# Kernel optimization log

Measured on AMD Instinct MI355X. Metric: run time of the kernel, lower is better.

## Reference

```python
import jax, jax.numpy as jnp
import numpy as np
import math

ITERATIONS = 2
STRIDE = 1
ALPHA = 0.0
MEAN_DATA = 1.0
FINAL_LAMBDA = 0.01  # final_beta
EPS = 1e-7
MIN_VAR_ADD = 0.0005


def setup_inputs() -> dict:
    key = jax.random.key(0)
    k1, k2 = jax.random.split(key)
    b, h, w, k, i, o, a = 2, 12, 12, 3, 32, 32, 4
    votes = jax.random.normal(k1, (b, h, w, k, k, i, o, a, a), dtype=jnp.float32)
    acts = jax.random.uniform(k2, (b, h, w, k, k, i, 1, 1, 1), dtype=jnp.float32)
    beta_a = jnp.full((1, 1, 1, 1, 1, 1, o, 1, 1), 0.5, dtype=jnp.float32)
    beta_u = jnp.full((1, 1, 1, 1, 1, 1, o, 1, 1), 0.5, dtype=jnp.float32)
    return {"votes": votes, "acts": acts, "beta_a": beta_a, "beta_u": beta_u}


def reference(votes, acts, beta_a, beta_u):
    b, h, w, k = votes.shape[0], votes.shape[1], votes.shape[2], votes.shape[3]
    i, o, a = votes.shape[5], votes.shape[6], votes.shape[7]
    s = STRIDE
    Hr = h * s + k - s  # reconstructed height
    Wr = w * s + k - s
    # target spatial coords for each (h,y) / (w,x) of the kernel window
    Y = jnp.arange(h)[:, None] * s + jnp.arange(k)[None, :]  # (h,k)
    X = jnp.arange(w)[:, None] * s + jnp.arange(k)[None, :]  # (w,k)
    lin = (Y[:, None, :, None] * Wr + X[None, :, None, :]).reshape(-1)  # (h*w*k*k,)

    # R_ij init: softmax over zeros along out-capsule axis -> uniform 1/o
    R = jnp.full((b, h, w, k, k, i, o, 1, 1), 1.0 / o, dtype=votes.dtype)
    out_poses = jnp.zeros((b, h, w, 1, 1, 1, o, a, a), dtype=votes.dtype)

    def m_step(R, out_poses, it):
        Ra = R * acts                                   # (b,h,w,k,k,i,o,1,1)
        sumR = jnp.sum(Ra, axis=(3, 4, 5), keepdims=True)
        mu = jnp.sum(Ra * votes, axis=(3, 4, 5), keepdims=True) / (sumR + EPS)
        mu = (1.0 - ALPHA) * mu + ALPHA * out_poses     # (b,h,w,1,1,1,o,a,a)
        sig = jnp.sum(Ra * jnp.square(votes - mu), axis=(3, 4, 5), keepdims=True) / (sumR + EPS) + MIN_VAR_ADD
        cost = (beta_u - 0.5 * jnp.log(sig + EPS)) * sumR / MEAN_DATA
        inv_temp = FINAL_LAMBDA * (1.0 - 0.95 ** (it + 1))
        a_j = jax.nn.sigmoid(inv_temp * (beta_a - jnp.sum(cost, axis=(-1, -2), keepdims=True)))
        return mu, sig, a_j

    def e_step(mu, sig, a_j):
        log_p = -jnp.sum(jnp.log(2.0 * math.pi * sig) + jnp.square(votes - mu) / (2.0 * sig),
                         axis=(-1, -2), keepdims=True)        # (b,h,w,k,k,i,o,1,1)
        lognum = jnp.log(a_j) + log_p
        ap = jnp.exp(lognum - jnp.max(lognum))                # global-max shift as in original
        # scatter-add (fold / col2im) onto the reconstructed grid, then sum over o
        ap6 = ap.reshape(b, h, w, k, k, i, o)
        ap_t = ap6.transpose(1, 2, 3, 4, 0, 5, 6).reshape(h * w * k * k, b, i, o)
        dense = jax.ops.segment_sum(ap_t, lin, num_segments=Hr * Wr)  # (Hr*Wr,b,i,o)
        dense = dense.sum(-1).reshape(Hr, Wr, b, i)
        # extract_patches: gather the window sums back to (b,h,w,k,k,i)
        denom = dense[Y[:, None, :, None], X[None, :, None, :]]  # (h,w,k,k,b,i)
        denom = jnp.transpose(denom, (4, 0, 1, 2, 3, 5))[..., None, None, None]
        return ap / (denom + EPS)

    for it in range(ITERATIONS - 1):
        mu, sig, a_j = m_step(R, out_poses, it)
        out_poses = mu
        R = e_step(mu, sig, a_j)
    mu, sig, a_j = m_step(R, out_poses, ITERATIONS)

    poses = jnp.squeeze(mu, axis=(3, 4, 5))     # (b,h,w,o,a,a)
    acts_out = jnp.squeeze(a_j, axis=(3, 4, 5))  # (b,h,w,o,1,1)
    return poses, acts_out
```

## Files before the change

### kernel.cpp

```cpp
#include <hip/hip_runtime.h>
#include <math.h>

#define NB 2
#define NH 12
#define NW 12
#define NK 3
#define NI 32
#define NO 32
#define NA 16
#define NBHW (NB*NH*NW)
#define NC (NK*NK*NI)
#define CSTR (NO*NA)
#define VPB (NC*CSTR)
#define HR 14
#define WR 14
#define EPSF 1e-7f
#define MINVAR 5e-4f
#define TEMP0 0.0005f
#define TEMPF 0.00142625f

#define MU_OFF 0
#define W_OFF  147456
#define L_OFF  294912
#define BM_OFF 304128
#define M_OFF  304416
#define DENSE_OFF 304432
#define LOGNUM_OFF 316976
#define DENSE_N (NB*HR*WR*NI)

__global__ __launch_bounds__(256) void kA(const float* __restrict__ votes,
        const float* __restrict__ acts, const float* __restrict__ beta_a,
        const float* __restrict__ beta_u, float* __restrict__ ws) {
    __shared__ float s_acts[NC];
    const int bid = blockIdx.x;
    const int bhw = bid >> 1;
    const int obase = (bid & 1) * 16;
    const int t = threadIdx.x;
    const int a = t & 15;
    const int o = obase + (t >> 4);
    for (int idx = t; idx < NC; idx += 256) s_acts[idx] = acts[bhw*NC + idx];
    __syncthreads();
    const float* vb = votes + (size_t)bhw*VPB + obase*NA;
    float s1 = 0.f, s2 = 0.f, sumR = 0.f;
    #pragma unroll 4
    for (int c = 0; c < NC; ++c) {
        float v  = vb[(size_t)c*CSTR + t];
        float ra = s_acts[c] * (1.0f/NO);
        float rv = ra * v;
        s1 += rv;
        s2 = fmaf(rv, v, s2);
        sumR += ra;
    }
    float mu  = s1 / (sumR + EPSF);
    float sig = (s2 - mu*(2.f*s1 - mu*sumR)) / (sumR + EPSF) + MINVAR;
    ws[MU_OFF + bhw*512 + a*32 + o] = mu;
    ws[W_OFF  + bhw*512 + a*32 + o] = 0.5f / sig;
    float cost = (beta_u[o] - 0.5f*logf(sig + EPSF)) * sumR;
    float ps   = logf(6.2831853071795864f * sig);
    #pragma unroll
    for (int d = 1; d < 16; d <<= 1) {
        cost += __shfl_xor(cost, d);
        ps   += __shfl_xor(ps, d);
    }
    if (a == 0) {
        float aj = 1.0f/(1.0f + expf(-TEMP0*(beta_a[o] - cost)));
        ws[L_OFF + bhw*32 + o] = logf(aj) - ps;
    }
}

__global__ __launch_bounds__(256) void kB(const float* __restrict__ votes,
                                          float* __restrict__ ws) {
    const int bhw = blockIdx.x;
    const int t = threadIdx.x;
    const int o = t & 31;
    float mur[16], wr[16];
    const float* mup = ws + MU_OFF + bhw*512;
    const float* wp  = ws + W_OFF  + bhw*512;
    #pragma unroll
    for (int a = 0; a < 16; ++a) { mur[a] = mup[a*32+o]; wr[a] = wp[a*32+o]; }
    const float L = ws[L_OFF + bhw*32 + o];
    const float* vb = votes + (size_t)bhw*VPB;
    float* lp = ws + LOGNUM_OFF + (size_t)bhw*(NC*NO);
    float tmax = -3.0e38f;
    for (int it = 0; it < (NC*NO)/256/32*32/ (32/32); ) { break; }
    for (int it = 0; it < 36; ++it) {
        const int c = it*8 + (t >> 5);
        const float4* v4 = (const float4*)(vb + (size_t)c*CSTR + o*NA);
        float acc = 0.f;
        #pragma unroll
        for (int q = 0; q < 4; ++q) {
            float4 v = v4[q];
            float d0 = v.x - mur[q*4+0]; acc = fmaf(d0*d0, wr[q*4+0], acc);
            float d1 = v.y - mur[q*4+1]; acc = fmaf(d1*d1, wr[q*4+1], acc);
            float d2 = v.z - mur[q*4+2]; acc = fmaf(d2*d2, wr[q*4+2], acc);
            float d3 = v.w - mur[q*4+3]; acc = fmaf(d3*d3, wr[q*4+3], acc);
        }
        float ln = L - acc;
        lp[c*32 + o] = ln;
        tmax = fmaxf(tmax, ln);
    }
    #pragma unroll
    for (int d = 1; d < 64; d <<= 1) tmax = fmaxf(tmax, __shfl_xor(tmax, d));
    __shared__ float smax[4];
    if ((t & 63) == 0) smax[t >> 6] = tmax;
    __syncthreads();
    if (t == 0)
        ws[BM_OFF + bhw] = fmaxf(fmaxf(smax[0], smax[1]), fmaxf(smax[2], smax[3]));
}

__global__ __launch_bounds__(256) void kBmax(float* __restrict__ ws) {
    const int t = threadIdx.x;
    float m = -3.0e38f;
    for (int i = t; i < NBHW; i += 256) m = fmaxf(m, ws[BM_OFF + i]);
    #pragma unroll
    for (int d = 1; d < 64; d <<= 1) m = fmaxf(m, __shfl_xor(m, d));
    __shared__ float sm[4];
    if ((t & 63) == 0) sm[t >> 6] = m;
    __syncthreads();
    if (t == 0) ws[M_OFF] = fmaxf(fmaxf(sm[0], sm[1]), fmaxf(sm[2], sm[3]));
}

__global__ __launch_bounds__(256) void kC(float* __restrict__ ws) {
    const int bhw = blockIdx.x;
    const int t = threadIdx.x;
    const int b = bhw / (NH*NW);
    const int rem = bhw % (NH*NW);
    const int y = rem / NW, x = rem % NW;
    const float M = ws[M_OFF];
    const float* lp = ws + LOGNUM_OFF + (size_t)bhw*(NC*NO);
    float* dense = ws + DENSE_OFF;
    for (int c = t; c < NC; c += 256) {
        const float* l = lp + c*32;
        float s = 0.f;
        #pragma unroll
        for (int o = 0; o < 32; ++o) s += expf(l[o] - M);
        const int i = c & 31, kk = c >> 5;
        const int ky = kk / 3, kx = kk % 3;
        atomicAdd(&dense[((b*HR + y+ky)*WR + (x+kx))*NI + i], s);
    }
}

__global__ __launch_bounds__(256) void kD(const float* __restrict__ votes,
        const float* __restrict__ acts, const float* __restrict__ beta_a,
        const float* __restrict__ beta_u, const float* __restrict__ ws,
        float* __restrict__ out) {
    __shared__ float s_rd[NC];
    const int bid = blockIdx.x;
    const int bhw = bid >> 1;
    const int obase = (bid & 1) * 16;
    const int t = threadIdx.x;
    const int a = t & 15;
    const int o = obase + (t >> 4);
    const int b = bhw / (NH*NW);
    const int rem = bhw % (NH*NW);
    const int y = rem / NW, x = rem % NW;
    const float* dense = ws + DENSE_OFF;
    for (int c = t; c < NC; c += 256) {
        const int i = c & 31, kk = c >> 5;
        const int ky = kk / 3, kx = kk % 3;
        float dn = dense[((b*HR + y+ky)*WR + (x+kx))*NI + i];
        s_rd[c] = acts[bhw*NC + c] / (dn + EPSF);
    }
    __syncthreads();
    const float M = ws[M_OFF];
    const float* lp = ws + LOGNUM_OFF + (size_t)bhw*(NC*NO) + o;
    const float* vb = votes + (size_t)bhw*VPB + obase*NA;
    float s1 = 0.f, s2 = 0.f, sumR = 0.f;
    #pragma unroll 4
    for (int c = 0; c < NC; ++c) {
        float ap = expf(lp[c*32] - M);
        float ra = s_rd[c] * ap;
        float v  = vb[(size_t)c*CSTR + t];
        float rv = ra * v;
        s1 += rv;
        s2 = fmaf(rv, v, s2);
        sumR += ra;
    }
    float mu  = s1 / (sumR + EPSF);
    float sig = (s2 - mu*(2.f*s1 - mu*sumR)) / (sumR + EPSF) + MINVAR;
    out[bhw*512 + obase*16 + t] = mu;
    float cost = (beta_u[o] - 0.5f*logf(sig + EPSF)) * sumR;
    #pragma unroll
    for (int d = 1; d < 16; d <<= 1) cost += __shfl_xor(cost, d);
    if (a == 0) {
        float aj = 1.0f/(1.0f + expf(-TEMPF*(beta_a[o] - cost)));
        out[NBHW*512 + bhw*32 + o] = aj;
    }
}

extern "C" void kernel_launch(void* const* d_in, const int* in_sizes, int n_in,
                              void* d_out, int out_size, void* d_ws, size_t ws_size,
                              hipStream_t stream) {
    const float* votes  = (const float*)d_in[0];
    const float* acts   = (const float*)d_in[1];
    const float* beta_a = (const float*)d_in[2];
    const float* beta_u = (const float*)d_in[3];
    float* ws  = (float*)d_ws;
    float* out = (float*)d_out;

    hipMemsetAsync(ws + DENSE_OFF, 0, DENSE_N*sizeof(float), stream);
    kA   <<<NBHW*2, 256, 0, stream>>>(votes, acts, beta_a, beta_u, ws);
    kB   <<<NBHW,   256, 0, stream>>>(votes, ws);
    kBmax<<<1,      256, 0, stream>>>(ws);
    kC   <<<NBHW,   256, 0, stream>>>(ws);
    kD   <<<NBHW*2, 256, 0, stream>>>(votes, acts, beta_a, beta_u, ws, out);
}
```

Measured before the change: 322.9 us.

## Split child-capsule reductions across more blocks with atomic partial sums

```diff
diff --git a/kernel.cpp b/kernel.cpp
--- a/kernel.cpp
+++ b/kernel.cpp
@@ -19,38 +19,74 @@
 #define TEMP0 0.0005f
 #define TEMPF 0.00142625f
 
-#define MU_OFF 0
-#define W_OFF  147456
-#define L_OFF  294912
-#define BM_OFF 304128
-#define M_OFF  304416
-#define DENSE_OFF 304432
-#define LOGNUM_OFF 316976
+#define CH 8
+#define CPC (NC/CH)
+#define ITERS (CPC/2)
+
+#define A_S1 0
+#define A_S2 147456
+#define A_SR 294912
+#define D_S1 295200
+#define D_S2 442656
+#define D_SR 590112
+#define DENSE_OFF 599328
+#define BM_OFF 611872
+#define ZERO_N 614176
+#define MU_OFF 614176
+#define W_OFF  761632
+#define L_OFF  909088
+#define M_OFF  918304
+#define LOGNUM_OFF 918308
 #define DENSE_N (NB*HR*WR*NI)
 
 __global__ __launch_bounds__(256) void kA(const float* __restrict__ votes,
-        const float* __restrict__ acts, const float* __restrict__ beta_a,
+        const float* __restrict__ acts, float* __restrict__ ws) {
+    __shared__ float s_acts[CPC];
+    const int bid = blockIdx.x;
+    const int bhw = bid >> 3;
+    const int cbase = (bid & 7) * CPC;
+    const int t = threadIdx.x;
+    if (t < CPC) s_acts[t] = acts[bhw*NC + cbase + t] * (1.0f/NO);
+    __syncthreads();
+    const int child_sub = t >> 7;
+    const int rem = t & 127;
+    const int o = rem >> 2;
+    const int quad = rem & 3;
+    const float4* vb4 = (const float4*)votes + (size_t)bhw*(VPB/4);
+    float s1[4] = {0,0,0,0}, s2[4] = {0,0,0,0};
+    float sumR = 0.f;
+    #pragma unroll 6
+    for (int it = 0; it < ITERS; ++it) {
+        const int c_loc = it*2 + child_sub;
+        float4 v = vb4[(size_t)(cbase + c_loc)*128 + rem];
+        float ra = s_acts[c_loc];
+        s1[0] += ra*v.x; s2[0] = fmaf(ra*v.x, v.x, s2[0]);
+        s1[1] += ra*v.y; s2[1] = fmaf(ra*v.y, v.y, s2[1]);
+        s1[2] += ra*v.z; s2[2] = fmaf(ra*v.z, v.z, s2[2]);
+        s1[3] += ra*v.w; s2[3] = fmaf(ra*v.w, v.w, s2[3]);
+        sumR += ra;
+    }
+    const int base = bhw*512 + o*16 + quad*4;
+    #pragma unroll
+    for (int j = 0; j < 4; ++j) {
+        atomicAdd(&ws[A_S1 + base + j], s1[j]);
+        atomicAdd(&ws[A_S2 + base + j], s2[j]);
+    }
+    if (rem == 0) atomicAdd(&ws[A_SR + bhw], sumR);
+}
+
+__global__ __launch_bounds__(256) void kA2(const float* __restrict__ beta_a,
         const float* __restrict__ beta_u, float* __restrict__ ws) {
-    __shared__ float s_acts[NC];
     const int bid = blockIdx.x;
     const int bhw = bid >> 1;
     const int obase = (bid & 1) * 16;
     const int t = threadIdx.x;
     const int a = t & 15;
     const int o = obase + (t >> 4);
-    for (int idx = t; idx < NC; idx += 256) s_acts[idx] = acts[bhw*NC + idx];
-    __syncthreads();
-    const float* vb = votes + (size_t)bhw*VPB + obase*NA;
-    float s1 = 0.f, s2 = 0.f, sumR = 0.f;
-    #pragma unroll 4
-    for (int c = 0; c < NC; ++c) {
-        float v  = vb[(size_t)c*CSTR + t];
-        float ra = s_acts[c] * (1.0f/NO);
-        float rv = ra * v;
-        s1 += rv;
-        s2 = fmaf(rv, v, s2);
-        sumR += ra;
-    }
+    const int idx = bhw*512 + o*16 + a;
+    float s1 = ws[A_S1 + idx];
+    float s2 = ws[A_S2 + idx];
+    float sumR = ws[A_SR + bhw];
     float mu  = s1 / (sumR + EPSF);
     float sig = (s2 - mu*(2.f*s1 - mu*sumR)) / (sumR + EPSF) + MINVAR;
     ws[MU_OFF + bhw*512 + a*32 + o] = mu;
@@ -70,33 +106,37 @@
 
 __global__ __launch_bounds__(256) void kB(const float* __restrict__ votes,
                                           float* __restrict__ ws) {
-    const int bhw = blockIdx.x;
-    const int t = threadIdx.x;
-    const int o = t & 31;
-    float mur[16], wr[16];
-    const float* mup = ws + MU_OFF + bhw*512;
-    const float* wp  = ws + W_OFF  + bhw*512;
-    #pragma unroll
-    for (int a = 0; a < 16; ++a) { mur[a] = mup[a*32+o]; wr[a] = wp[a*32+o]; }
+    const int bid = blockIdx.x;
+    const int bhw = bid >> 3;
+    const int cbase = (bid & 7) * CPC;
+    const int t = threadIdx.x;
+    const int child_sub = t >> 7;
+    const int rem = t & 127;
+    const int o = rem >> 2;
+    const int quad = rem & 3;
+    float mur[4], wr[4];
+    #pragma unroll
+    for (int j = 0; j < 4; ++j) {
+        mur[j] = ws[MU_OFF + bhw*512 + (quad*4+j)*32 + o];
+        wr[j]  = ws[W_OFF  + bhw*512 + (quad*4+j)*32 + o];
+    }
     const float L = ws[L_OFF + bhw*32 + o];
-    const float* vb = votes + (size_t)bhw*VPB;
+    const float4* vb4 = (const float4*)votes + (size_t)bhw*(VPB/4);
     float* lp = ws + LOGNUM_OFF + (size_t)bhw*(NC*NO);
     float tmax = -3.0e38f;
-    for (int it = 0; it < (NC*NO)/256/32*32/ (32/32); ) { break; }
-    for (int it = 0; it < 36; ++it) {
-        const int c = it*8 + (t >> 5);
-        const float4* v4 = (const float4*)(vb + (size_t)c*CSTR + o*NA);
-        float acc = 0.f;
-        #pragma unroll
-        for (int q = 0; q < 4; ++q) {
-            float4 v = v4[q];
-            float d0 = v.x - mur[q*4+0]; acc = fmaf(d0*d0, wr[q*4+0], acc);
-            float d1 = v.y - mur[q*4+1]; acc = fmaf(d1*d1, wr[q*4+1], acc);
-            float d2 = v.z - mur[q*4+2]; acc = fmaf(d2*d2, wr[q*4+2], acc);
-            float d3 = v.w - mur[q*4+3]; acc = fmaf(d3*d3, wr[q*4+3], acc);
-        }
+    #pragma unroll 6
+    for (int it = 0; it < ITERS; ++it) {
+        const int c = cbase + it*2 + child_sub;
+        float4 v = vb4[(size_t)c*128 + rem];
+        float d0 = v.x - mur[0];
+        float acc = d0*d0*wr[0];
+        float d1 = v.y - mur[1]; acc = fmaf(d1*d1, wr[1], acc);
+        float d2 = v.z - mur[2]; acc = fmaf(d2*d2, wr[2], acc);
+        float d3 = v.w - mur[3]; acc = fmaf(d3*d3, wr[3], acc);
+        acc += __shfl_xor(acc, 1);
+        acc += __shfl_xor(acc, 2);
         float ln = L - acc;
-        lp[c*32 + o] = ln;
+        if (quad == 0) lp[c*32 + o] = ln;
         tmax = fmaxf(tmax, ln);
     }
     #pragma unroll
@@ -105,13 +145,13 @@
     if ((t & 63) == 0) smax[t >> 6] = tmax;
     __syncthreads();
     if (t == 0)
-        ws[BM_OFF + bhw] = fmaxf(fmaxf(smax[0], smax[1]), fmaxf(smax[2], smax[3]));
+        ws[BM_OFF + bid] = fmaxf(fmaxf(smax[0], smax[1]), fmaxf(smax[2], smax[3]));
 }
 
 __global__ __launch_bounds__(256) void kBmax(float* __restrict__ ws) {
     const int t = threadIdx.x;
     float m = -3.0e38f;
-    for (int i = t; i < NBHW; i += 256) m = fmaxf(m, ws[BM_OFF + i]);
+    for (int i = t; i < NBHW*CH; i += 256) m = fmaxf(m, ws[BM_OFF + i]);
     #pragma unroll
     for (int d = 1; d < 64; d <<= 1) m = fmaxf(m, __shfl_xor(m, d));
     __shared__ float sm[4];
@@ -121,7 +161,9 @@
 }
 
 __global__ __launch_bounds__(256) void kC(float* __restrict__ ws) {
-    const int bhw = blockIdx.x;
+    const int bid = blockIdx.x;
+    const int bhw = bid >> 2;
+    const int cbase = (bid & 3) * 72;
     const int t = threadIdx.x;
     const int b = bhw / (NH*NW);
     const int rem = bhw % (NH*NW);
@@ -129,53 +171,85 @@
     const float M = ws[M_OFF];
     const float* lp = ws + LOGNUM_OFF + (size_t)bhw*(NC*NO);
     float* dense = ws + DENSE_OFF;
-    for (int c = t; c < NC; c += 256) {
-        const float* l = lp + c*32;
-        float s = 0.f;
+    const int o = t & 31;
+    for (int it = 0; it < 9; ++it) {
+        const int c = cbase + it*8 + (t >> 5);
+        float s = expf(lp[c*32 + o] - M);
         #pragma unroll
-        for (int o = 0; o < 32; ++o) s += expf(l[o] - M);
+        for (int d = 1; d < 32; d <<= 1) s += __shfl_xor(s, d);
+        if (o == 0) {
+            const int i = c & 31, kk = c >> 5;
+            const int ky = kk / 3, kx = kk % 3;
+            atomicAdd(&dense[((b*HR + y+ky)*WR + (x+kx))*NI + i], s);
+        }
+    }
+}
+
+__global__ __launch_bounds__(256) void kD(const float* __restrict__ votes,
+        const float* __restrict__ acts, float* __restrict__ ws) {
+    __shared__ float s_rd[CPC];
+    __shared__ float s_ra[CPC*NO];
+    const int bid = blockIdx.x;
+    const int bhw = bid >> 3;
+    const int cbase = (bid & 7) * CPC;
+    const int t = threadIdx.x;
+    const int b = bhw / (NH*NW);
+    const int remhw = bhw % (NH*NW);
+    const int y = remhw / NW, x = remhw % NW;
+    if (t < CPC) {
+        const int c = cbase + t;
         const int i = c & 31, kk = c >> 5;
         const int ky = kk / 3, kx = kk % 3;
-        atomicAdd(&dense[((b*HR + y+ky)*WR + (x+kx))*NI + i], s);
-    }
-}
-
-__global__ __launch_bounds__(256) void kD(const float* __restrict__ votes,
-        const float* __restrict__ acts, const float* __restrict__ beta_a,
+        float dn = ws[DENSE_OFF + ((b*HR + y+ky)*WR + (x+kx))*NI + i];
+        s_rd[t] = acts[bhw*NC + c] / (dn + EPSF);
+    }
+    __syncthreads();
+    const float M = ws[M_OFF];
+    const float* lp = ws + LOGNUM_OFF + (size_t)bhw*(NC*NO) + (size_t)cbase*32;
+    for (int idx = t; idx < CPC*NO; idx += 256) {
+        s_ra[idx] = s_rd[idx >> 5] * expf(lp[idx] - M);
+    }
+    __syncthreads();
+    const int child_sub = t >> 7;
+    const int rem = t & 127;
+    const int o = rem >> 2;
+    const int quad = rem & 3;
+    const float4* vb4 = (const float4*)votes + (size_t)bhw*(VPB/4);
+    float s1[4] = {0,0,0,0}, s2[4] = {0,0,0,0};
+    float sumR = 0.f;
+    #pragma unroll 6
+    for (int it = 0; it < ITERS; ++it) {
+        const int c_loc = it*2 + child_sub;
+        float4 v = vb4[(size_t)(cbase + c_loc)*128 + rem];
+        float ra = s_ra[c_loc*32 + o];
+        s1[0] += ra*v.x; s2[0] = fmaf(ra*v.x, v.x, s2[0]);
+        s1[1] += ra*v.y; s2[1] = fmaf(ra*v.y, v.y, s2[1]);
+        s1[2] += ra*v.z; s2[2] = fmaf(ra*v.z, v.z, s2[2]);
+        s1[3] += ra*v.w; s2[3] = fmaf(ra*v.w, v.w, s2[3]);
+        sumR += ra;
+    }
+    const int base = bhw*512 + o*16 + quad*4;
+    #pragma unroll
+    for (int j = 0; j < 4; ++j) {
+        atomicAdd(&ws[D_S1 + base + j], s1[j]);
+        atomicAdd(&ws[D_S2 + base + j], s2[j]);
+    }
+    if (quad == 0) atomicAdd(&ws[D_SR + bhw*32 + o], sumR);
+}
+
+__global__ __launch_bounds__(256) void kD2(const float* __restrict__ beta_a,
         const float* __restrict__ beta_u, const float* __restrict__ ws,
         float* __restrict__ out) {
-    __shared__ float s_rd[NC];
     const int bid = blockIdx.x;
     const int bhw = bid >> 1;
     const int obase = (bid & 1) * 16;
     const int t = threadIdx.x;
     const int a = t & 15;
     const int o = obase + (t >> 4);
-    const int b = bhw / (NH*NW);
-    const int rem = bhw % (NH*NW);
-    const int y = rem / NW, x = rem % NW;
-    const float* dense = ws + DENSE_OFF;
-    for (int c = t; c < NC; c += 256) {
-        const int i = c & 31, kk = c >> 5;
-        const int ky = kk / 3, kx = kk % 3;
-        float dn = dense[((b*HR + y+ky)*WR + (x+kx))*NI + i];
-        s_rd[c] = acts[bhw*NC + c] / (dn + EPSF);
-    }
-    __syncthreads();
-    const float M = ws[M_OFF];
-    const float* lp = ws + LOGNUM_OFF + (size_t)bhw*(NC*NO) + o;
-    const float* vb = votes + (size_t)bhw*VPB + obase*NA;
-    float s1 = 0.f, s2 = 0.f, sumR = 0.f;
-    #pragma unroll 4
-    for (int c = 0; c < NC; ++c) {
-        float ap = expf(lp[c*32] - M);
-        float ra = s_rd[c] * ap;
-        float v  = vb[(size_t)c*CSTR + t];
-        float rv = ra * v;
-        s1 += rv;
-        s2 = fmaf(rv, v, s2);
-        sumR += ra;
-    }
+    const int idx = bhw*512 + o*16 + a;
+    float s1 = ws[D_S1 + idx];
+    float s2 = ws[D_S2 + idx];
+    float sumR = ws[D_SR + bhw*32 + o];
     float mu  = s1 / (sumR + EPSF);
     float sig = (s2 - mu*(2.f*s1 - mu*sumR)) / (sumR + EPSF) + MINVAR;
     out[bhw*512 + obase*16 + t] = mu;
@@ -198,10 +272,12 @@
     float* ws  = (float*)d_ws;
     float* out = (float*)d_out;
 
-    hipMemsetAsync(ws + DENSE_OFF, 0, DENSE_N*sizeof(float), stream);
-    kA   <<<NBHW*2, 256, 0, stream>>>(votes, acts, beta_a, beta_u, ws);
-    kB   <<<NBHW,   256, 0, stream>>>(votes, ws);
-    kBmax<<<1,      256, 0, stream>>>(ws);
-    kC   <<<NBHW,   256, 0, stream>>>(ws);
-    kD   <<<NBHW*2, 256, 0, stream>>>(votes, acts, beta_a, beta_u, ws, out);
-}
+    hipMemsetAsync(ws, 0, ZERO_N*sizeof(float), stream);
+    kA   <<<NBHW*CH, 256, 0, stream>>>(votes, acts, ws);
+    kA2  <<<NBHW*2,  256, 0, stream>>>(beta_a, beta_u, ws);
+    kB   <<<NBHW*CH, 256, 0, stream>>>(votes, ws);
+    kBmax<<<1,       256, 0, stream>>>(ws);
+    kC   <<<NBHW*4,  256, 0, stream>>>(ws);
+    kD   <<<NBHW*CH, 256, 0, stream>>>(votes, acts, ws);
+    kD2  <<<NBHW*2,  256, 0, stream>>>(beta_a, beta_u, ws, out);
+}
```

Result: slower. 382.5 us (+18.5%).
